# Performance work log

Measured on AMD Instinct MI355X. Metric: run time of the kernel, lower is better.

## Reference

```python
import jax, jax.numpy as jnp
import numpy as np

B, S, D, V = 64, 128, 64, 50000

def _prelu(x, a):
    return jnp.where(x >= 0, x, a * x)

def setup_inputs() -> dict:
    key = jax.random.key(0)
    ks = jax.random.split(key, 24)
    stdv = 1.0 / np.sqrt(D)
    u = lambda k, shape: jax.random.uniform(k, shape, jnp.float32, -stdv, stdv)
    emb = u(ks[0], (V, D)).at[0].set(0.0)  # padding_idx=0
    inp = {
        'items': jax.random.randint(ks[1], (B, S), 0, V),
        'A': jax.random.randint(ks[2], (B, S, S), 0, 2),
        'edgeorder': jax.random.randint(ks[3], (B, S, S), 0, S),
        'last_nodes': jax.random.randint(ks[4], (B,), 0, S),
        'mask': jnp.ones((B, S), dtype=bool),
        'emb': emb,
        'W_self': u(ks[5], (D, D)), 'W_neigh': u(ks[6], (D, D)),
        'prelu1': jnp.full((D,), 0.25, jnp.float32),
        'Wq': u(ks[7], (D, D)), 'bq': jnp.zeros((D,), jnp.float32),
        'Wk': u(ks[8], (D, D)), 'Wv': u(ks[9], (D, D)), 'we': u(ks[10], (D,)),
        'prelu2': jnp.full((D,), 0.25, jnp.float32),
        'Wu': u(ks[11], (D, D)), 'bu': jnp.zeros((D,), jnp.float32),
        'Wvr': u(ks[12], (D, D)), 'wer': u(ks[13], (D,)),
        'prelu3': jnp.full((D,), 0.25, jnp.float32),
        'W_sr': u(ks[14], (2 * D, D)),
    }
    return inp

def reference(items, A, edgeorder, last_nodes, mask, emb, W_self, W_neigh, prelu1,
              Wq, bq, Wk, Wv, we, prelu2, Wu, bu, Wvr, wer, prelu3, W_sr):
    x = emb[items]  # [B,S,D]
    # ---- EOPA: masked neighbor broadcast + edgeorder gather + max-pool ----
    adjT = (jnp.swapaxes(A, 1, 2) == 1)  # [B,S(target),S(neighbor)]
    neigh = jnp.where((adjT & mask[:, None, :])[..., None], x[:, None, :, :], 0.0)  # [B,S,S,D]
    eo_t = jnp.swapaxes(edgeorder, 1, 2)  # [B,S,S]
    # gathered[b,i,j,:] = neigh[b, edgeorder[b,j,i], j, :]
    neigh = jnp.take_along_axis(neigh, eo_t[..., None], axis=1)
    neigh = neigh.max(axis=2)  # [B,S,D]
    h = _prelu(x @ W_self + neigh @ W_neigh, prelu1)
    # ---- SGAT: sigmoid-gated attention over adjacency ----
    q = h @ Wq + bq
    k = h @ Wk
    v = h @ Wv
    e = k[:, :, None, :] + q[:, None, :, :]             # e[b,i,j,d]
    e = jnp.where((A == 1)[..., None], e, 0.0)
    e = jax.nn.sigmoid(e) @ we                           # [B,S,S]
    a = jax.nn.softmax(e, axis=1)                        # softmax over source i
    h2 = _prelu(jnp.einsum('bij,bid->bjd', a, v), prelu2)
    # ---- AttnReadout ----
    xu = h2 @ Wu + bu                                    # [B,S,D]
    xlast = h2[jnp.arange(h2.shape[0]), last_nodes]      # [B,D]
    xv = xlast @ Wvr
    eatt = jax.nn.sigmoid(xu + xv[:, None, :]) @ wer     # [B,S]
    alpha = jax.nn.softmax(eatt, axis=1)
    out = _prelu((h2 * alpha[..., None]).sum(axis=1), prelu3)  # [B,D]
    # ---- session representation ----
    sr = jnp.concatenate([out, xlast], axis=-1) @ W_sr   # [B,D]
    return sr
```

## Files before the change

kernel.cpp:

```cpp
#include <hip/hip_runtime.h>

#define BB 64
#define SS 128
#define DD 64
#define SSQ (SS*SS)
#define BSD (BB*SS*DD)

__device__ __forceinline__ float fast_sigmoid(float x) {
  return __builtin_amdgcn_rcpf(1.0f + __expf(-x));
}

__global__ __launch_bounds__(256) void kA(
    const int* __restrict__ items, const int* __restrict__ Aadj,
    const int* __restrict__ eo, const float* __restrict__ emb,
    const float* __restrict__ Wself, const float* __restrict__ Wneigh,
    const float* __restrict__ prelu1,
    const float* __restrict__ Wq, const float* __restrict__ bq,
    const float* __restrict__ Wk, const float* __restrict__ Wv,
    float* __restrict__ q_ws, float* __restrict__ k_ws, float* __restrict__ v_ws)
{
  __shared__ alignas(16) float xs[SS*DD];
  __shared__ alignas(16) float Wb[2][DD*DD];
  __shared__ alignas(16) float nms[16*DD];
  __shared__ alignas(16) float hs[16*DD];
  __shared__ unsigned short condw[SS];
  const int b  = blockIdx.x >> 3;
  const int i0 = (blockIdx.x & 7) * 16;
  const int tid = threadIdx.x;
  const int wv = tid >> 6, lane = tid & 63;

  {
    const float4* emb4 = (const float4*)emb;
    float4* xs4 = (float4*)xs;
    for (int f = tid; f < SS*16; f += 256) {
      int j = f >> 4, qd = f & 15;
      xs4[f] = emb4[items[b*SS + j]*16 + qd];
    }
    const float4* W4 = (const float4*)Wself;
    float4* Wb4 = (float4*)Wb[0];
    for (int f = tid; f < 1024; f += 256) Wb4[f] = W4[f];
  }
  {
    int eov[8];
#pragma unroll
    for (int k = 0; k < 8; k++) {
      int p = tid + k*256;
      eov[k] = eo[b*SSQ + (p >> 4)*SS + i0 + (p & 15)];
    }
#pragma unroll
    for (int k = 0; k < 8; k++) {
      int p = tid + k*256;
      bool c = (Aadj[b*SSQ + (p >> 4)*SS + eov[k]] == 1);
      unsigned long long bm = __ballot(c);
      if ((lane & 15) == 0)
        condw[p >> 4] = (unsigned short)(bm >> lane);
    }
  }
  __syncthreads();

  {
    const float4* W4 = (const float4*)Wneigh;
    float4* Wb4 = (float4*)Wb[1];
    for (int f = tid; f < 1024; f += 256) Wb4[f] = W4[f];
  }
  {
    float m[4];
#pragma unroll
    for (int t = 0; t < 4; t++) m[t] = -__builtin_inff();
    for (int j = 0; j < SS; j++) {
      unsigned int cw = (unsigned int)condw[j] >> (wv*4);
      float xv = xs[j*DD + lane];
#pragma unroll
      for (int t = 0; t < 4; t++) {
        float val = ((cw >> t) & 1u) ? xv : 0.0f;
        m[t] = fmaxf(m[t], val);
      }
    }
#pragma unroll
    for (int t = 0; t < 4; t++) nms[(wv*4 + t)*DD + lane] = m[t];
  }
  float acc[4];
#pragma unroll
  for (int t = 0; t < 4; t++) acc[t] = 0.0f;
  for (int kk = 0; kk < DD; kk++) {
    float w = Wb[0][kk*DD + lane];
#pragma unroll
    for (int t = 0; t < 4; t++)
      acc[t] = fmaf(xs[(i0 + wv*4 + t)*DD + kk], w, acc[t]);
  }
  __syncthreads();

  {
    const float4* W4 = (const float4*)Wq;
    float4* Wb4 = (float4*)Wb[0];
    for (int f = tid; f < 1024; f += 256) Wb4[f] = W4[f];
  }
  for (int kk = 0; kk < DD; kk++) {
    float w = Wb[1][kk*DD + lane];
#pragma unroll
    for (int t = 0; t < 4; t++)
      acc[t] = fmaf(nms[(wv*4 + t)*DD + kk], w, acc[t]);
  }
  {
    float p1 = prelu1[lane];
#pragma unroll
    for (int t = 0; t < 4; t++) {
      float h = acc[t];
      hs[(wv*4 + t)*DD + lane] = (h >= 0.0f) ? h : p1*h;
    }
  }
  __syncthreads();

  const int r0g = b*SS + i0;
  {
    const float4* W4 = (const float4*)Wk;
    float4* Wb4 = (float4*)Wb[1];
    for (int f = tid; f < 1024; f += 256) Wb4[f] = W4[f];
  }
  {
    float bqv = bq[lane];
#pragma unroll
    for (int t = 0; t < 4; t++) acc[t] = bqv;
    for (int kk = 0; kk < DD; kk++) {
      float w = Wb[0][kk*DD + lane];
#pragma unroll
      for (int t = 0; t < 4; t++)
        acc[t] = fmaf(hs[(wv*4 + t)*DD + kk], w, acc[t]);
    }
#pragma unroll
    for (int t = 0; t < 4; t++) q_ws[(r0g + wv*4 + t)*DD + lane] = acc[t];
  }
  __syncthreads();

  {
    const float4* W4 = (const float4*)Wv;
    float4* Wb4 = (float4*)Wb[0];
    for (int f = tid; f < 1024; f += 256) Wb4[f] = W4[f];
  }
  {
#pragma unroll
    for (int t = 0; t < 4; t++) acc[t] = 0.0f;
    for (int kk = 0; kk < DD; kk++) {
      float w = Wb[1][kk*DD + lane];
#pragma unroll
      for (int t = 0; t < 4; t++)
        acc[t] = fmaf(hs[(wv*4 + t)*DD + kk], w, acc[t]);
    }
#pragma unroll
    for (int t = 0; t < 4; t++) k_ws[(r0g + wv*4 + t)*DD + lane] = acc[t];
  }
  __syncthreads();

  {
#pragma unroll
    for (int t = 0; t < 4; t++) acc[t] = 0.0f;
    for (int kk = 0; kk < DD; kk++) {
      float w = Wb[0][kk*DD + lane];
#pragma unroll
      for (int t = 0; t < 4; t++)
        acc[t] = fmaf(hs[(wv*4 + t)*DD + kk], w, acc[t]);
    }
#pragma unroll
    for (int t = 0; t < 4; t++) v_ws[(r0g + wv*4 + t)*DD + lane] = acc[t];
  }
}

__global__ __launch_bounds__(256) void kB(
    const int* __restrict__ Aadj,
    const float* __restrict__ q_ws, const float* __restrict__ k_ws,
    const float* __restrict__ v_ws,
    const float* __restrict__ we, const float* __restrict__ prelu2,
    const float* __restrict__ Wu, const float* __restrict__ bu,
    float* __restrict__ h2_ws, float* __restrict__ xu_ws)
{
  __shared__ alignas(16) float ks[SS*65];
  __shared__ alignas(16) float qs[16*65];
  __shared__ alignas(16) float es[16*129];
  __shared__ float wes[DD];
  const int b  = blockIdx.x >> 3;
  const int j0 = (blockIdx.x & 7) * 16;
  const int tid = threadIdx.x;
  const int wv = tid >> 6, lane = tid & 63;

  {
    const float4* k4 = (const float4*)k_ws;
    for (int f = tid; f < 2048; f += 256) {
      int i = f >> 4, d4 = f & 15;
      float4 v = k4[(b*SS + i)*16 + d4];
      float* dst = &ks[i*65 + d4*4];
      dst[0] = v.x; dst[1] = v.y; dst[2] = v.z; dst[3] = v.w;
    }
    const float4* q4 = (const float4*)q_ws;
    for (int f = tid; f < 256; f += 256) {
      int jl = f >> 4, d4 = f & 15;
      float4 v = q4[(b*SS + j0 + jl)*16 + d4];
      float* dst = &qs[jl*65 + d4*4];
      dst[0] = v.x; dst[1] = v.y; dst[2] = v.z; dst[3] = v.w;
    }
  }
  if (tid < DD) wes[tid] = we[tid];
  float hw = we[lane];
  for (int off = 32; off >= 1; off >>= 1) hw += __shfl_xor(hw, off);
  const float half_sum = 0.5f * hw;
  __syncthreads();

#pragma unroll
  for (int k = 0; k < 8; k++) {
    int p = tid + k*256;
    int jl = p & 15, i = p >> 4;
    float e2;
    if (Aadj[b*SSQ + i*SS + j0 + jl] == 1) {
      float s = 0.0f;
      for (int d2 = 0; d2 < DD; d2++) {
        float t = ks[i*65 + d2] + qs[jl*65 + d2];
        s = fmaf(wes[d2], fast_sigmoid(t), s);
      }
      e2 = s;
    } else {
      e2 = half_sum;
    }
    es[jl*129 + i] = e2;
  }
  __syncthreads();

  float* vs = ks;
  {
    const float4* v4 = (const float4*)v_ws;
    float4* vs4 = (float4*)vs;
    for (int f = tid; f < 2048; f += 256)
      vs4[f] = v4[b*SS*16 + f];
  }
#pragma unroll
  for (int t = 0; t < 4; t++) {
    int jl = wv*4 + t;
    float a0 = es[jl*129 + lane], a1 = es[jl*129 + 64 + lane];
    float mx = fmaxf(a0, a1);
    for (int off = 32; off >= 1; off >>= 1) mx = fmaxf(mx, __shfl_xor(mx, off));
    float p0 = __expf(a0 - mx), p1 = __expf(a1 - mx);
    float sm = p0 + p1;
    for (int off = 32; off >= 1; off >>= 1) sm += __shfl_xor(sm, off);
    float inv = 1.0f / sm;
    es[jl*129 + lane]      = p0 * inv;
    es[jl*129 + 64 + lane] = p1 * inv;
  }
  __syncthreads();

  float acc[4];
#pragma unroll
  for (int t = 0; t < 4; t++) acc[t] = 0.0f;
  for (int i = 0; i < SS; i++) {
    float vv = vs[i*DD + lane];
#pragma unroll
    for (int t = 0; t < 4; t++)
      acc[t] = fmaf(es[(wv*4 + t)*129 + i], vv, acc[t]);
  }
  float h2r[4];
  {
    float p2 = prelu2[lane];
#pragma unroll
    for (int t = 0; t < 4; t++) {
      float h2 = acc[t];
      h2r[t] = (h2 >= 0.0f) ? h2 : p2*h2;
      h2_ws[(b*SS + j0 + wv*4 + t)*DD + lane] = h2r[t];
    }
  }
  __syncthreads();

  float* hs2 = es;
  float* Wus = ks;
#pragma unroll
  for (int t = 0; t < 4; t++) hs2[(wv*4 + t)*DD + lane] = h2r[t];
  {
    const float4* W4 = (const float4*)Wu;
    float4* Wus4 = (float4*)Wus;
    for (int f = tid; f < 1024; f += 256) Wus4[f] = W4[f];
  }
  __syncthreads();
  {
    float buv = bu[lane];
    float acc2[4];
#pragma unroll
    for (int t = 0; t < 4; t++) acc2[t] = buv;
    for (int kk = 0; kk < DD; kk++) {
      float w = Wus[kk*DD + lane];
#pragma unroll
      for (int t = 0; t < 4; t++)
        acc2[t] = fmaf(hs2[(wv*4 + t)*DD + kk], w, acc2[t]);
    }
#pragma unroll
    for (int t = 0; t < 4; t++)
      xu_ws[(b*SS + j0 + wv*4 + t)*DD + lane] = acc2[t];
  }
}

__global__ __launch_bounds__(512) void k4_readout(
    const float* __restrict__ h2_ws, const float* __restrict__ xu_ws,
    const int* __restrict__ last_nodes,
    const float* __restrict__ Wvr, const float* __restrict__ wer,
    const float* __restrict__ prelu3, const float* __restrict__ Wsr,
    float* __restrict__ out)
{
  __shared__ float xlast[DD], xv[DD], eatt[SS], alpha[SS], outs[DD];
  __shared__ float pools[8*DD];
  const int b = blockIdx.x;
  const int tid = threadIdx.x;
  const int wv = tid >> 6, lane = tid & 63;

  const int ln = last_nodes[b];
  if (tid < DD) xlast[tid] = h2_ws[(b*SS + ln)*DD + tid];
  __syncthreads();
  if (tid < DD) {
    float s = 0.0f;
    for (int k2 = 0; k2 < DD; k2++)
      s = fmaf(xlast[k2], Wvr[k2*DD + tid], s);
    xv[tid] = s;
  }
  __syncthreads();
  {
    float werv = wer[lane];
    float xvl = xv[lane];
    for (int j = wv; j < SS; j += 8) {
      float xuv = xu_ws[(b*SS + j)*DD + lane];
      float term = fast_sigmoid(xuv + xvl) * werv;
      for (int off = 32; off >= 1; off >>= 1) term += __shfl_xor(term, off);
      if (lane == 0) eatt[j] = term;
    }
  }
  __syncthreads();
  if (wv == 0) {
    float a0 = eatt[lane], a1 = eatt[64 + lane];
    float mx = fmaxf(a0, a1);
    for (int off = 32; off >= 1; off >>= 1) mx = fmaxf(mx, __shfl_xor(mx, off));
    float p0 = __expf(a0 - mx), p1 = __expf(a1 - mx);
    float sm = p0 + p1;
    for (int off = 32; off >= 1; off >>= 1) sm += __shfl_xor(sm, off);
    float inv = 1.0f / sm;
    alpha[lane]      = p0 * inv;
    alpha[64 + lane] = p1 * inv;
  }
  __syncthreads();
  {
    float part = 0.0f;
    for (int j = wv; j < SS; j += 8)
      part = fmaf(alpha[j], h2_ws[(b*SS + j)*DD + lane], part);
    pools[wv*DD + lane] = part;
  }
  __syncthreads();
  if (wv == 0) {
    float s = 0.0f;
#pragma unroll
    for (int w = 0; w < 8; w++) s += pools[w*DD + lane];
    float p3 = prelu3[lane];
    outs[lane] = (s >= 0.0f) ? s : p3 * s;
  }
  __syncthreads();
  {
    float fs = 0.0f;
    for (int m2 = wv*16; m2 < wv*16 + 16; m2++) {
      float src = (m2 < DD) ? outs[m2] : xlast[m2 - DD];
      fs = fmaf(src, Wsr[m2*DD + lane], fs);
    }
    pools[wv*DD + lane] = fs;
  }
  __syncthreads();
  if (wv == 0) {
    float s = 0.0f;
#pragma unroll
    for (int w = 0; w < 8; w++) s += pools[w*DD + lane];
    out[b*DD + lane] = s;
  }
}

extern "C" void kernel_launch(void* const* d_in, const int* in_sizes, int n_in,
                              void* d_out, int out_size, void* d_ws, size_t ws_size,
                              hipStream_t stream)
{
  const int* items = (const int*)d_in[0];
  const int* Aadj  = (const int*)d_in[1];
  const int* eo    = (const int*)d_in[2];
  const int* lastn = (const int*)d_in[3];
  const float* emb    = (const float*)d_in[5];
  const float* Wself  = (const float*)d_in[6];
  const float* Wneigh = (const float*)d_in[7];
  const float* p1     = (const float*)d_in[8];
  const float* Wq     = (const float*)d_in[9];
  const float* bq     = (const float*)d_in[10];
  const float* Wk     = (const float*)d_in[11];
  const float* Wv     = (const float*)d_in[12];
  const float* we     = (const float*)d_in[13];
  const float* p2     = (const float*)d_in[14];
  const float* Wu     = (const float*)d_in[15];
  const float* bu     = (const float*)d_in[16];
  const float* Wvr    = (const float*)d_in[17];
  const float* wer    = (const float*)d_in[18];
  const float* p3     = (const float*)d_in[19];
  const float* Wsr    = (const float*)d_in[20];

  float* ws    = (float*)d_ws;
  float* q_ws  = ws;
  float* k_ws  = ws + (size_t)BSD;
  float* v_ws  = ws + (size_t)2*BSD;
  float* h2_ws = ws + (size_t)3*BSD;
  float* xu_ws = ws + (size_t)4*BSD;

  kA<<<BB*8, 256, 0, stream>>>(items, Aadj, eo, emb, Wself, Wneigh, p1,
                               Wq, bq, Wk, Wv, q_ws, k_ws, v_ws);
  kB<<<BB*8, 256, 0, stream>>>(Aadj, q_ws, k_ws, v_ws, we, p2, Wu, bu,
                               h2_ws, xu_ws);
  k4_readout<<<BB, 512, 0, stream>>>(h2_ws, xu_ws, lastn, Wvr, wer, p3, Wsr,
                                     (float*)d_out);
}
```

Measured before the change: 184.5 us.

## Broadcast row operands via readlane instead of LDS staging in kA and kB

```diff
diff --git a/kernel.cpp b/kernel.cpp
--- a/kernel.cpp
+++ b/kernel.cpp
@@ -8,6 +8,9 @@
 
 __device__ __forceinline__ float fast_sigmoid(float x) {
   return __builtin_amdgcn_rcpf(1.0f + __expf(-x));
+}
+__device__ __forceinline__ float rl(float v, int l) {
+  return __int_as_float(__builtin_amdgcn_readlane(__float_as_int(v), l));
 }
 
 __global__ __launch_bounds__(256) void kA(
@@ -21,8 +24,6 @@
 {
   __shared__ alignas(16) float xs[SS*DD];
   __shared__ alignas(16) float Wb[2][DD*DD];
-  __shared__ alignas(16) float nms[16*DD];
-  __shared__ alignas(16) float hs[16*DD];
   __shared__ unsigned short condw[SS];
   const int b  = blockIdx.x >> 3;
   const int i0 = (blockIdx.x & 7) * 16;
@@ -63,30 +64,27 @@
     float4* Wb4 = (float4*)Wb[1];
     for (int f = tid; f < 1024; f += 256) Wb4[f] = W4[f];
   }
-  {
-    float m[4];
-#pragma unroll
-    for (int t = 0; t < 4; t++) m[t] = -__builtin_inff();
-    for (int j = 0; j < SS; j++) {
-      unsigned int cw = (unsigned int)condw[j] >> (wv*4);
-      float xv = xs[j*DD + lane];
-#pragma unroll
-      for (int t = 0; t < 4; t++) {
-        float val = ((cw >> t) & 1u) ? xv : 0.0f;
-        m[t] = fmaxf(m[t], val);
-      }
-    }
-#pragma unroll
-    for (int t = 0; t < 4; t++) nms[(wv*4 + t)*DD + lane] = m[t];
-  }
-  float acc[4];
-#pragma unroll
-  for (int t = 0; t < 4; t++) acc[t] = 0.0f;
+  float xrow[4], m[4], acc[4];
+#pragma unroll
+  for (int t = 0; t < 4; t++) {
+    xrow[t] = xs[(i0 + wv*4 + t)*DD + lane];
+    m[t] = -__builtin_inff();
+    acc[t] = 0.0f;
+  }
+  for (int j = 0; j < SS; j++) {
+    unsigned int cw = (unsigned int)condw[j] >> (wv*4);
+    float xv = xs[j*DD + lane];
+#pragma unroll
+    for (int t = 0; t < 4; t++) {
+      float val = ((cw >> t) & 1u) ? xv : 0.0f;
+      m[t] = fmaxf(m[t], val);
+    }
+  }
   for (int kk = 0; kk < DD; kk++) {
     float w = Wb[0][kk*DD + lane];
 #pragma unroll
     for (int t = 0; t < 4; t++)
-      acc[t] = fmaf(xs[(i0 + wv*4 + t)*DD + kk], w, acc[t]);
+      acc[t] = fmaf(rl(xrow[t], kk), w, acc[t]);
   }
   __syncthreads();
 
@@ -99,15 +97,14 @@
     float w = Wb[1][kk*DD + lane];
 #pragma unroll
     for (int t = 0; t < 4; t++)
-      acc[t] = fmaf(nms[(wv*4 + t)*DD + kk], w, acc[t]);
-  }
+      acc[t] = fmaf(rl(m[t], kk), w, acc[t]);
+  }
+  float hr[4];
   {
     float p1 = prelu1[lane];
 #pragma unroll
-    for (int t = 0; t < 4; t++) {
-      float h = acc[t];
-      hs[(wv*4 + t)*DD + lane] = (h >= 0.0f) ? h : p1*h;
-    }
+    for (int t = 0; t < 4; t++)
+      hr[t] = (acc[t] >= 0.0f) ? acc[t] : p1*acc[t];
   }
   __syncthreads();
 
@@ -119,16 +116,17 @@
   }
   {
     float bqv = bq[lane];
-#pragma unroll
-    for (int t = 0; t < 4; t++) acc[t] = bqv;
+    float a2[4];
+#pragma unroll
+    for (int t = 0; t < 4; t++) a2[t] = bqv;
     for (int kk = 0; kk < DD; kk++) {
       float w = Wb[0][kk*DD + lane];
 #pragma unroll
       for (int t = 0; t < 4; t++)
-        acc[t] = fmaf(hs[(wv*4 + t)*DD + kk], w, acc[t]);
-    }
-#pragma unroll
-    for (int t = 0; t < 4; t++) q_ws[(r0g + wv*4 + t)*DD + lane] = acc[t];
+        a2[t] = fmaf(rl(hr[t], kk), w, a2[t]);
+    }
+#pragma unroll
+    for (int t = 0; t < 4; t++) q_ws[(r0g + wv*4 + t)*DD + lane] = a2[t];
   }
   __syncthreads();
 
@@ -138,30 +136,32 @@
     for (int f = tid; f < 1024; f += 256) Wb4[f] = W4[f];
   }
   {
-#pragma unroll
-    for (int t = 0; t < 4; t++) acc[t] = 0.0f;
+    float a2[4];
+#pragma unroll
+    for (int t = 0; t < 4; t++) a2[t] = 0.0f;
     for (int kk = 0; kk < DD; kk++) {
       float w = Wb[1][kk*DD + lane];
 #pragma unroll
       for (int t = 0; t < 4; t++)
-        acc[t] = fmaf(hs[(wv*4 + t)*DD + kk], w, acc[t]);
-    }
-#pragma unroll
-    for (int t = 0; t < 4; t++) k_ws[(r0g + wv*4 + t)*DD + lane] = acc[t];
-  }
-  __syncthreads();
-
-  {
-#pragma unroll
-    for (int t = 0; t < 4; t++) acc[t] = 0.0f;
+        a2[t] = fmaf(rl(hr[t], kk), w, a2[t]);
+    }
+#pragma unroll
+    for (int t = 0; t < 4; t++) k_ws[(r0g + wv*4 + t)*DD + lane] = a2[t];
+  }
+  __syncthreads();
+
+  {
+    float a2[4];
+#pragma unroll
+    for (int t = 0; t < 4; t++) a2[t] = 0.0f;
     for (int kk = 0; kk < DD; kk++) {
       float w = Wb[0][kk*DD + lane];
 #pragma unroll
       for (int t = 0; t < 4; t++)
-        acc[t] = fmaf(hs[(wv*4 + t)*DD + kk], w, acc[t]);
-    }
-#pragma unroll
-    for (int t = 0; t < 4; t++) v_ws[(r0g + wv*4 + t)*DD + lane] = acc[t];
+        a2[t] = fmaf(rl(hr[t], kk), w, a2[t]);
+    }
+#pragma unroll
+    for (int t = 0; t < 4; t++) v_ws[(r0g + wv*4 + t)*DD + lane] = a2[t];
   }
 }
 
@@ -173,33 +173,35 @@
     const float* __restrict__ Wu, const float* __restrict__ bu,
     float* __restrict__ h2_ws, float* __restrict__ xu_ws)
 {
-  __shared__ alignas(16) float ks[SS*65];
-  __shared__ alignas(16) float qs[16*65];
+  __shared__ alignas(16) float ks[SS*68];
+  __shared__ alignas(16) float vs[SS*DD];
+  __shared__ alignas(16) float qs[16*68];
   __shared__ alignas(16) float es[16*129];
-  __shared__ float wes[DD];
   const int b  = blockIdx.x >> 3;
   const int j0 = (blockIdx.x & 7) * 16;
   const int tid = threadIdx.x;
   const int wv = tid >> 6, lane = tid & 63;
 
   {
-    const float4* k4 = (const float4*)k_ws;
+    const float4* k4p = (const float4*)k_ws;
+    float4* ks4 = (float4*)ks;
     for (int f = tid; f < 2048; f += 256) {
       int i = f >> 4, d4 = f & 15;
-      float4 v = k4[(b*SS + i)*16 + d4];
-      float* dst = &ks[i*65 + d4*4];
-      dst[0] = v.x; dst[1] = v.y; dst[2] = v.z; dst[3] = v.w;
-    }
-    const float4* q4 = (const float4*)q_ws;
-    for (int f = tid; f < 256; f += 256) {
-      int jl = f >> 4, d4 = f & 15;
-      float4 v = q4[(b*SS + j0 + jl)*16 + d4];
-      float* dst = &qs[jl*65 + d4*4];
-      dst[0] = v.x; dst[1] = v.y; dst[2] = v.z; dst[3] = v.w;
-    }
-  }
-  if (tid < DD) wes[tid] = we[tid];
-  float hw = we[lane];
+      ks4[i*17 + d4] = k4p[(b*SS + i)*16 + d4];
+    }
+    const float4* q4p = (const float4*)q_ws;
+    float4* qs4 = (float4*)qs;
+    if (tid < 256) {
+      int jl = tid >> 4, d4 = tid & 15;
+      qs4[jl*17 + d4] = q4p[(b*SS + j0 + jl)*16 + d4];
+    }
+    const float4* v4p = (const float4*)v_ws;
+    float4* vs4 = (float4*)vs;
+    for (int f = tid; f < 2048; f += 256)
+      vs4[f] = v4p[b*SS*16 + f];
+  }
+  float wrow = we[lane];
+  float hw = wrow;
   for (int off = 32; off >= 1; off >>= 1) hw += __shfl_xor(hw, off);
   const float half_sum = 0.5f * hw;
   __syncthreads();
@@ -212,8 +214,8 @@
     if (Aadj[b*SSQ + i*SS + j0 + jl] == 1) {
       float s = 0.0f;
       for (int d2 = 0; d2 < DD; d2++) {
-        float t = ks[i*65 + d2] + qs[jl*65 + d2];
-        s = fmaf(wes[d2], fast_sigmoid(t), s);
+        float t = ks[i*68 + d2] + qs[jl*68 + d2];
+        s = fmaf(rl(wrow, d2), fast_sigmoid(t), s);
       }
       e2 = s;
     } else {
@@ -223,13 +225,14 @@
   }
   __syncthreads();
 
-  float* vs = ks;
-  {
-    const float4* v4 = (const float4*)v_ws;
-    float4* vs4 = (float4*)vs;
-    for (int f = tid; f < 2048; f += 256)
-      vs4[f] = v4[b*SS*16 + f];
-  }
+  float* Wus = ks;
+  {
+    const float4* W4 = (const float4*)Wu;
+    float4* Wus4 = (float4*)Wus;
+    for (int f = tid; f < 1024; f += 256) Wus4[f] = W4[f];
+  }
+
+  float ar0[4], ar1[4];
 #pragma unroll
   for (int t = 0; t < 4; t++) {
     int jl = wv*4 + t;
@@ -240,19 +243,24 @@
     float sm = p0 + p1;
     for (int off = 32; off >= 1; off >>= 1) sm += __shfl_xor(sm, off);
     float inv = 1.0f / sm;
-    es[jl*129 + lane]      = p0 * inv;
-    es[jl*129 + 64 + lane] = p1 * inv;
-  }
-  __syncthreads();
+    ar0[t] = p0 * inv;
+    ar1[t] = p1 * inv;
+  }
 
   float acc[4];
 #pragma unroll
   for (int t = 0; t < 4; t++) acc[t] = 0.0f;
-  for (int i = 0; i < SS; i++) {
+  for (int i = 0; i < 64; i++) {
     float vv = vs[i*DD + lane];
 #pragma unroll
     for (int t = 0; t < 4; t++)
-      acc[t] = fmaf(es[(wv*4 + t)*129 + i], vv, acc[t]);
+      acc[t] = fmaf(rl(ar0[t], i), vv, acc[t]);
+  }
+  for (int i = 0; i < 64; i++) {
+    float vv = vs[(64 + i)*DD + lane];
+#pragma unroll
+    for (int t = 0; t < 4; t++)
+      acc[t] = fmaf(rl(ar1[t], i), vv, acc[t]);
   }
   float h2r[4];
   {
@@ -266,30 +274,20 @@
   }
   __syncthreads();
 
-  float* hs2 = es;
-  float* Wus = ks;
-#pragma unroll
-  for (int t = 0; t < 4; t++) hs2[(wv*4 + t)*DD + lane] = h2r[t];
-  {
-    const float4* W4 = (const float4*)Wu;
-    float4* Wus4 = (float4*)Wus;
-    for (int f = tid; f < 1024; f += 256) Wus4[f] = W4[f];
-  }
-  __syncthreads();
   {
     float buv = bu[lane];
-    float acc2[4];
-#pragma unroll
-    for (int t = 0; t < 4; t++) acc2[t] = buv;
+    float a2[4];
+#pragma unroll
+    for (int t = 0; t < 4; t++) a2[t] = buv;
     for (int kk = 0; kk < DD; kk++) {
       float w = Wus[kk*DD + lane];
 #pragma unroll
       for (int t = 0; t < 4; t++)
-        acc2[t] = fmaf(hs2[(wv*4 + t)*DD + kk], w, acc2[t]);
-    }
-#pragma unroll
-    for (int t = 0; t < 4; t++)
-      xu_ws[(b*SS + j0 + wv*4 + t)*DD + lane] = acc2[t];
+        a2[t] = fmaf(rl(h2r[t], kk), w, a2[t]);
+    }
+#pragma unroll
+    for (int t = 0; t < 4; t++)
+      xu_ws[(b*SS + j0 + wv*4 + t)*DD + lane] = a2[t];
   }
 }
 
```

Result: no change. 184.6 us (+0.0%).
